# Kernel optimization log

Measured on AMD Instinct MI355X. Metric: run time of the kernel, lower is better.

Reference implementation:

```python
import jax, jax.numpy as jnp
import numpy as np

E = 64          # num_routed_experts
K = 6           # num_experts_per_token
NS = 2          # num_shared_experts
D = 512         # hidden_size
F = 512         # expert_intermediate_size = intermediate_size // 4


def setup_inputs() -> dict:
    key = jax.random.key(0)
    ks = jax.random.split(key, 8)
    s = 0.02
    return {
        "hidden_states": jax.random.normal(ks[0], (2, 1024, D), dtype=jnp.float32),
        "Wr": jax.random.normal(ks[1], (D, E), dtype=jnp.float32) * s,      # router
        "sWg": jax.random.normal(ks[2], (NS, D, F), dtype=jnp.float32) * s,  # shared gate_proj
        "sWu": jax.random.normal(ks[3], (NS, D, F), dtype=jnp.float32) * s,  # shared up_proj
        "sWd": jax.random.normal(ks[4], (NS, F, D), dtype=jnp.float32) * s,  # shared down_proj
        "Wg": jax.random.normal(ks[5], (E, D, F), dtype=jnp.float32) * s,    # routed gate_proj
        "Wu": jax.random.normal(ks[6], (E, D, F), dtype=jnp.float32) * s,    # routed up_proj
        "Wd": jax.random.normal(ks[7], (E, F, D), dtype=jnp.float32) * s,    # routed down_proj
    }


def _swiglu_ffn(x, wg, wu, wd):
    # x: (N, D); wg/wu: (D, F); wd: (F, D)
    return (jax.nn.silu(x @ wg) * (x @ wu)) @ wd


def reference(hidden_states, Wr, sWg, sWu, sWd, Wg, Wu, Wd):
    B, S, d = hidden_states.shape
    x = hidden_states.reshape(-1, d)  # (N, D)
    N = x.shape[0]

    # ---- shared experts (always on) ----
    shared = jnp.zeros_like(x)
    for e in range(NS):
        shared = shared + _swiglu_ffn(x, sWg[e], sWu[e], sWd[e])

    # ---- top-k router ----
    logits = x @ Wr                                   # (N, E)
    probs = jax.nn.softmax(logits, axis=-1)
    top_w, top_i = jax.lax.top_k(probs, K)            # (N, K)
    top_w = top_w / jnp.sum(top_w, axis=-1, keepdims=True)  # renormalize
    gate = jnp.zeros((N, E), dtype=x.dtype).at[jnp.arange(N)[:, None], top_i].set(top_w)

    # ---- routed experts: per-expert FFN, combined with sparse gate ----
    routed = jnp.zeros_like(x)
    for e in range(E):
        routed = routed + _swiglu_ffn(x, Wg[e], Wu[e], Wd[e]) * gate[:, e:e + 1]

    out = (shared + routed + x).reshape(B, S, d)
    return out
```

## Files before the change

### kernel.cpp

```cpp
#include <hip/hip_runtime.h>

#define N_TOK 2048
#define DD 512
#define FF 512
#define EE 64
#define TK 6
#define NG 66
#define RSLOT 12288
#define NSLOT 16384
#define BM 64
#define BN 64
#define NT 16
#define MAXT 320

typedef float f32x4 __attribute__((ext_vector_type(4)));
typedef __bf16 bf16x8 __attribute__((ext_vector_type(8)));

__device__ __forceinline__ unsigned cvtpk(float lo, float hi) {
  unsigned r;
  asm("v_cvt_pk_bf16_f32 %0, %1, %2" : "=v"(r) : "v"(lo), "v"(hi));
  return r;
}

__device__ __forceinline__ bf16x8 pack8(f32x4 a, f32x4 b) {
  union { unsigned u[4]; bf16x8 v; } r;
  r.u[0] = cvtpk(a[0], a[1]); r.u[1] = cvtpk(a[2], a[3]);
  r.u[2] = cvtpk(b[0], b[1]); r.u[3] = cvtpk(b[2], b[3]);
  return r.v;
}

__device__ __forceinline__ void gll16(const void* g, void* l) {
  __builtin_amdgcn_global_load_lds(
      (const __attribute__((address_space(1))) unsigned int*)g,
      (__attribute__((address_space(3))) unsigned int*)l, 16, 0, 0);
}

__global__ __launch_bounds__(256) void router_k(
    const float* __restrict__ x, const float* __restrict__ Wr,
    int* __restrict__ top_i, float* __restrict__ top_w, int* __restrict__ cnt) {
  __shared__ float xs[16 * 512];
  __shared__ float part[4][16][64];
  int tid = threadIdx.x, lane = tid & 63, w = tid >> 6;
  int t0 = blockIdx.x * 16;

  const f32x4* xin = (const f32x4*)(x + (size_t)t0 * DD);
  f32x4* xs4 = (f32x4*)xs;
#pragma unroll
  for (int i = 0; i < 8; ++i) xs4[i * 256 + tid] = xin[i * 256 + tid];
  __syncthreads();

  float acc[16];
#pragma unroll
  for (int t = 0; t < 16; ++t) acc[t] = 0.f;
  for (int kk = 0; kk < 32; ++kk) {
    int k = w * 128 + kk * 4;
    float w0 = Wr[(size_t)(k + 0) * EE + lane];
    float w1 = Wr[(size_t)(k + 1) * EE + lane];
    float w2 = Wr[(size_t)(k + 2) * EE + lane];
    float w3 = Wr[(size_t)(k + 3) * EE + lane];
#pragma unroll
    for (int t = 0; t < 16; ++t) {
      f32x4 xv = *(const f32x4*)&xs[t * 512 + k];
      acc[t] = fmaf(xv[0], w0, acc[t]);
      acc[t] = fmaf(xv[1], w1, acc[t]);
      acc[t] = fmaf(xv[2], w2, acc[t]);
      acc[t] = fmaf(xv[3], w3, acc[t]);
    }
  }
#pragma unroll
  for (int t = 0; t < 16; ++t) part[w][t][lane] = acc[t];
  __syncthreads();

#pragma unroll
  for (int tt = 0; tt < 4; ++tt) {
    int t = w * 4 + tt;
    float l0 = part[0][t][lane] + part[1][t][lane] + part[2][t][lane] + part[3][t][lane];
    float m = l0;
#pragma unroll
    for (int s = 32; s; s >>= 1) m = fmaxf(m, __shfl_xor(m, s));
    float p = __expf(l0 - m);
    int wi[TK]; float wv[TK];
#pragma unroll
    for (int it = 0; it < TK; ++it) {
      float v = p;
#pragma unroll
      for (int s = 32; s; s >>= 1) v = fmaxf(v, __shfl_xor(v, s));
      unsigned long long b = __ballot(p == v);
      int idx = __ffsll((unsigned long long)b) - 1;
      wi[it] = idx; wv[it] = v;
      if (lane == idx) p = -1.f;
    }
    float wsum = 0.f;
#pragma unroll
    for (int it = 0; it < TK; ++it) wsum += wv[it];
    int tg = t0 + t;
    if (lane < TK) {
      int si = 0; float sv = 0.f;
#pragma unroll
      for (int it = 0; it < TK; ++it) if (lane == it) { si = wi[it]; sv = wv[it]; }
      top_i[tg * TK + lane] = si;
      top_w[tg * TK + lane] = sv / wsum;
      atomicAdd(&cnt[si], 1);
    }
  }
}

__global__ void offsets_k(const int* __restrict__ cnt, int* __restrict__ goff,
                          int* __restrict__ fill, int* __restrict__ wk_g,
                          int* __restrict__ wk_mt, int* __restrict__ nitems) {
  int i = threadIdx.x;
  fill[i] = 0;
  int c = cnt[i];
  int s = c;
#pragma unroll
  for (int d = 1; d < 64; d <<= 1) { int t = __shfl_up(s, d); if (i >= d) s += t; }
  goff[i] = s - c;
  if (i == 63) {
    goff[EE] = RSLOT;
    goff[EE + 1] = RSLOT + N_TOK;
    goff[EE + 2] = RSLOT + 2 * N_TOK;
  }
  int nt = (c + BM - 1) >> 6;
  int ts = nt;
#pragma unroll
  for (int d = 1; d < 64; d <<= 1) { int t = __shfl_up(ts, d); if (i >= d) ts += t; }
  int texcl = ts - nt;
  for (int t = 0; t < nt; ++t) { wk_g[texcl + t] = i; wk_mt[texcl + t] = t; }
  int tot = __shfl(ts, 63);
  wk_g[tot + i] = EE + (i >> 5);
  wk_mt[tot + i] = i & 31;
  if (i == 0) nitems[0] = tot + 64;
}

__global__ void scatter_k(const int* __restrict__ top_i, const float* __restrict__ top_w,
                          const int* __restrict__ goff, int* __restrict__ fill,
                          int* __restrict__ btok, float* __restrict__ bw) {
  int idx = blockIdx.x * blockDim.x + threadIdx.x;
  if (idx < RSLOT) {
    int e = top_i[idx];
    int pos = goff[e] + atomicAdd(&fill[e], 1);
    btok[pos] = idx / TK;
    bw[pos] = top_w[idx];
  } else if (idx < NSLOT) {
    int j = idx - RSLOT;
    btok[idx] = j & (N_TOK - 1);
    bw[idx] = 1.0f;
  }
}

__global__ void initout_k(const float* __restrict__ x, float* __restrict__ out, int n4) {
  int i = blockIdx.x * blockDim.x + threadIdx.x;
  if (i < n4) reinterpret_cast<f32x4*>(out)[i] = reinterpret_cast<const f32x4*>(x)[i];
}

__global__ __launch_bounds__(256) void gemm1_k(
    const float* __restrict__ x, const float* __restrict__ Wg, const float* __restrict__ Wu,
    const float* __restrict__ sWg, const float* __restrict__ sWu,
    const int* __restrict__ goff, const int* __restrict__ btok,
    const int* __restrict__ wk_g, const int* __restrict__ wk_mt,
    const int* __restrict__ nitems,
    short* __restrict__ H) {
  int item = blockIdx.y;
  if (item >= nitems[0]) return;
  int g = wk_g[item], mt = wk_mt[item];
  int s0g = goff[g], cnt = goff[g + 1] - s0g;
  int n0 = blockIdx.x * BN;
  const float* wgp = (g < EE) ? Wg + (size_t)g * DD * FF : sWg + (size_t)(g - EE) * DD * FF;
  const float* wup = (g < EE) ? Wu + (size_t)g * DD * FF : sWu + (size_t)(g - EE) * DD * FF;

  __shared__ __align__(16) float lds[2][6144];

  int tid = threadIdx.x;
  int lane = tid & 63;
  int w = tid >> 6;
  int wr = w >> 1, wc = w & 1;
  int lr = lane & 15, lgq = lane >> 4;
  int s0 = s0g + mt * BM;

  const float* sp[6];
  int ldsoff[6], strf[6];
#pragma unroll
  for (int q = 0; q < 6; ++q) {
    int c = w * 6 + q;
    ldsoff[q] = c * 256;
    if (c < 8) {
      int row = c * 8 + (lane >> 3);
      int tok = btok[s0 + row];
      sp[q] = x + (size_t)tok * DD + (((lane & 7) ^ (lane >> 3)) << 2);
      strf[q] = 32;
    } else if (c < 16) {
      int cc = c - 8;
      int krow = cc * 4 + (lane >> 4);
      int colf = ((((lane & 15) << 4) ^ (((cc >> 1) & 3) << 5)) >> 2);
      sp[q] = wgp + (size_t)krow * FF + n0 + colf;
      strf[q] = 32 * FF;
    } else {
      int cc = c - 16;
      int krow = cc * 4 + (lane >> 4);
      int colf = ((((lane & 15) << 4) ^ (((cc >> 1) & 3) << 5)) >> 2);
      sp[q] = wup + (size_t)krow * FF + n0 + colf;
      strf[q] = 32 * FF;
    }
  }

  f32x4 accg[2][2], accu[2][2];
#pragma unroll
  for (int i = 0; i < 2; ++i)
#pragma unroll
    for (int j = 0; j < 2; ++j) {
      accg[i][j] = f32x4{0.f, 0.f, 0.f, 0.f};
      accu[i][j] = f32x4{0.f, 0.f, 0.f, 0.f};
    }

  auto STAGE = [&](int b, int kt) {
#pragma unroll
    for (int q = 0; q < 6; ++q)
      gll16(sp[q] + (size_t)kt * strf[q], &lds[b][ldsoff[q]]);
  };
  auto COMPUTE = [&](int b) {
    const float* Am = &lds[b][0];
    const float* Gm = &lds[b][2048];
    const float* Um = &lds[b][4096];
    bf16x8 af[2], bg[2], bu[2];
#pragma unroll
    for (int i = 0; i < 2; ++i) {
      int row = wr * 32 + i * 16 + lr;
      int sw = (row & 7) << 2;
      f32x4 v0 = *(const f32x4*)&Am[row * 32 + ((lgq * 8) ^ sw)];
      f32x4 v1 = *(const f32x4*)&Am[row * 32 + ((lgq * 8 + 4) ^ sw)];
      af[i] = pack8(v0, v1);
    }
#pragma unroll
    for (int j = 0; j < 2; ++j) {
      int col = wc * 32 + j * 16 + lr;
      int cx = col ^ (lgq << 3);
      int kb = lgq * 8;
      f32x4 g0, g1, u0, u1;
#pragma unroll
      for (int i2 = 0; i2 < 4; ++i2) {
        g0[i2] = Gm[(kb + i2) * 64 + cx];
        g1[i2] = Gm[(kb + 4 + i2) * 64 + cx];
        u0[i2] = Um[(kb + i2) * 64 + cx];
        u1[i2] = Um[(kb + 4 + i2) * 64 + cx];
      }
      bg[j] = pack8(g0, g1);
      bu[j] = pack8(u0, u1);
    }
#pragma unroll
    for (int i = 0; i < 2; ++i)
#pragma unroll
      for (int j = 0; j < 2; ++j) {
        accg[i][j] = __builtin_amdgcn_mfma_f32_16x16x32_bf16(af[i], bg[j], accg[i][j], 0, 0, 0);
        accu[i][j] = __builtin_amdgcn_mfma_f32_16x16x32_bf16(af[i], bu[j], accu[i][j], 0, 0, 0);
      }
  };

  STAGE(0, 0);
  __syncthreads();
  int b = 0;
#pragma unroll 1
  for (int kt = 0; kt < NT; ++kt) {
    if (kt + 1 < NT) STAGE(b ^ 1, kt + 1);
    COMPUTE(b);
    __syncthreads();
    b ^= 1;
  }

#pragma unroll
  for (int i = 0; i < 2; ++i)
#pragma unroll
    for (int j = 0; j < 2; ++j)
#pragma unroll
      for (int r = 0; r < 4; ++r) {
        int mrow = wr * 32 + i * 16 + lgq * 4 + r;
        if (mt * BM + mrow < cnt) {
          float gg = accg[i][j][r];
          float uu = accu[i][j][r];
          float hv = (gg / (1.f + __expf(-gg))) * uu;
          int col = n0 + wc * 32 + j * 16 + lr;
          H[(size_t)(s0 + mrow) * FF + col] = (short)(cvtpk(hv, hv) & 0xffffu);
        }
      }
}

__global__ __launch_bounds__(256) void gemm2_k(
    const short* __restrict__ H, const float* __restrict__ Wd, const float* __restrict__ sWd,
    const int* __restrict__ goff, const int* __restrict__ btok, const float* __restrict__ bw,
    const int* __restrict__ wk_g, const int* __restrict__ wk_mt,
    const int* __restrict__ nitems,
    float* __restrict__ out) {
  int item = blockIdx.y;
  if (item >= nitems[0]) return;
  int g = wk_g[item], mt = wk_mt[item];
  int s0g = goff[g], cnt = goff[g + 1] - s0g;
  int n0 = blockIdx.x * BN;
  const float* wdp = (g < EE) ? Wd + (size_t)g * FF * DD : sWd + (size_t)(g - EE) * FF * DD;

  __shared__ __align__(16) short lds[2][6144];

  int tid = threadIdx.x;
  int lane = tid & 63;
  int w = tid >> 6;
  int wr = w >> 1, wc = w & 1;
  int lr = lane & 15, lgq = lane >> 4;
  int s0 = s0g + mt * BM;

  const char* sp[3];
  int ldsbyte[3], strb[3];
#pragma unroll
  for (int q = 0; q < 3; ++q) {
    int c = w * 3 + q;
    ldsbyte[q] = c * 1024;
    if (c < 4) {
      int row = c * 16 + (lane >> 2);
      int slot = s0 + row;
      sp[q] = (const char*)(H + (size_t)slot * FF + (((lane & 3) ^ ((lane >> 2) & 3)) << 3));
      strb[q] = 64;
    } else {
      int cc = c - 4;
      int krow = cc * 4 + (lane >> 4);
      int colf = ((((lane & 15) << 4) ^ (((cc >> 1) & 3) << 5)) >> 2);
      sp[q] = (const char*)(wdp + (size_t)krow * DD + n0 + colf);
      strb[q] = 32 * DD * 4;
    }
  }

  f32x4 acc[2][2];
#pragma unroll
  for (int i = 0; i < 2; ++i)
#pragma unroll
    for (int j = 0; j < 2; ++j) acc[i][j] = f32x4{0.f, 0.f, 0.f, 0.f};

  auto STAGE = [&](int b, int kt) {
#pragma unroll
    for (int q = 0; q < 3; ++q)
      gll16(sp[q] + (size_t)kt * strb[q], (char*)lds[b] + ldsbyte[q]);
  };
  auto COMPUTE = [&](int b) {
    const short* Hm = lds[b];
    const float* Bm = (const float*)(lds[b] + 2048);
    bf16x8 af[2], bd[2];
#pragma unroll
    for (int i = 0; i < 2; ++i) {
      int row = wr * 32 + i * 16 + lr;
      af[i] = *(const bf16x8*)&Hm[row * 32 + ((lgq * 8) ^ ((row & 3) << 3))];
    }
#pragma unroll
    for (int j = 0; j < 2; ++j) {
      int col = wc * 32 + j * 16 + lr;
      int cx = col ^ (lgq << 3);
      int kb = lgq * 8;
      f32x4 d0, d1;
#pragma unroll
      for (int i2 = 0; i2 < 4; ++i2) {
        d0[i2] = Bm[(kb + i2) * 64 + cx];
        d1[i2] = Bm[(kb + 4 + i2) * 64 + cx];
      }
      bd[j] = pack8(d0, d1);
    }
#pragma unroll
    for (int i = 0; i < 2; ++i)
#pragma unroll
      for (int j = 0; j < 2; ++j)
        acc[i][j] = __builtin_amdgcn_mfma_f32_16x16x32_bf16(af[i], bd[j], acc[i][j], 0, 0, 0);
  };

  STAGE(0, 0);
  __syncthreads();
  int b = 0;
#pragma unroll 1
  for (int kt = 0; kt < NT; ++kt) {
    if (kt + 1 < NT) STAGE(b ^ 1, kt + 1);
    COMPUTE(b);
    __syncthreads();
    b ^= 1;
  }

#pragma unroll
  for (int i = 0; i < 2; ++i)
#pragma unroll
    for (int r = 0; r < 4; ++r) {
      int mrow = wr * 32 + i * 16 + lgq * 4 + r;
      if (mt * BM + mrow < cnt) {
        int slot = s0 + mrow;
        int tok = btok[slot];
        float wv = bw[slot];
#pragma unroll
        for (int j = 0; j < 2; ++j) {
          int col = n0 + wc * 32 + j * 16 + lr;
          atomicAdd(&out[(size_t)tok * DD + col], acc[i][j][r] * wv);
        }
      }
    }
}

extern "C" void kernel_launch(void* const* d_in, const int* in_sizes, int n_in,
                              void* d_out, int out_size, void* d_ws, size_t ws_size,
                              hipStream_t stream) {
  const float* x   = (const float*)d_in[0];
  const float* Wr  = (const float*)d_in[1];
  const float* sWg = (const float*)d_in[2];
  const float* sWu = (const float*)d_in[3];
  const float* sWd = (const float*)d_in[4];
  const float* Wg  = (const float*)d_in[5];
  const float* Wu  = (const float*)d_in[6];
  const float* Wd  = (const float*)d_in[7];
  float* out = (float*)d_out;

  char* wsb = (char*)d_ws;
  size_t off = 0;
  short* H = (short*)(wsb + off);     off += (size_t)NSLOT * FF * 2;
  int*   top_i = (int*)(wsb + off);   off += (size_t)RSLOT * 4;
  float* top_w = (float*)(wsb + off); off += (size_t)RSLOT * 4;
  int*   btok = (int*)(wsb + off);    off += (size_t)NSLOT * 4;
  float* bwt  = (float*)(wsb + off);  off += (size_t)NSLOT * 4;
  int*   cnt  = (int*)(wsb + off);    off += 256;
  int*   fill = (int*)(wsb + off);    off += 256;
  int*   goff = (int*)(wsb + off);    off += 512;
  int*   wk_g = (int*)(wsb + off);    off += MAXT * 4;
  int*   wk_mt = (int*)(wsb + off);   off += MAXT * 4;
  int*   nitems = (int*)(wsb + off);  off += 256;

  hipMemsetAsync(cnt, 0, 256, stream);
  router_k<<<N_TOK / 16, 256, 0, stream>>>(x, Wr, top_i, top_w, cnt);
  offsets_k<<<1, 64, 0, stream>>>(cnt, goff, fill, wk_g, wk_mt, nitems);
  scatter_k<<<NSLOT / 256, 256, 0, stream>>>(top_i, top_w, goff, fill, btok, bwt);
  int n4 = out_size / 4;
  initout_k<<<(n4 + 255) / 256, 256, 0, stream>>>(x, out, n4);
  dim3 grid1(FF / BN, MAXT, 1);
  gemm1_k<<<grid1, 256, 0, stream>>>(x, Wg, Wu, sWg, sWu, goff, btok, wk_g, wk_mt, nitems, H);
  dim3 grid2(DD / BN, MAXT, 1);
  gemm2_k<<<grid2, 256, 0, stream>>>(H, Wd, sWd, goff, btok, bwt, wk_g, wk_mt, nitems, out);
}
```

Measured before the change: 196.9 us.

## Pre-convert weights and activations to transposed bf16 before grouped GEMMs

Adds per-call kernels that convert all expert weight matrices to bf16 in an N-major transposed layout, and the input x to bf16. The GEMM kernels then stage bf16 tiles directly into LDS with K=64 per stage and swizzled 16-byte reads, so the per-element fp32 loads and in-loop packing are gone. This halves GEMM operand bytes and simplifies the LDS fragment loads. In exchange, every call runs an extra pass that reads all ~200 MB of fp32 weights and writes 100 MB of bf16, which is likely to dominate the runtime.

```diff
diff --git a/kernel.cpp b/kernel.cpp
--- a/kernel.cpp
+++ b/kernel.cpp
@@ -10,8 +10,10 @@
 #define NSLOT 16384
 #define BM 64
 #define BN 64
-#define NT 16
+#define BK 64
+#define NKT 8
 #define MAXT 320
+#define MATSZ 262144
 
 typedef float f32x4 __attribute__((ext_vector_type(4)));
 typedef __bf16 bf16x8 __attribute__((ext_vector_type(8)));
@@ -22,17 +24,54 @@
   return r;
 }
 
-__device__ __forceinline__ bf16x8 pack8(f32x4 a, f32x4 b) {
-  union { unsigned u[4]; bf16x8 v; } r;
-  r.u[0] = cvtpk(a[0], a[1]); r.u[1] = cvtpk(a[2], a[3]);
-  r.u[2] = cvtpk(b[0], b[1]); r.u[3] = cvtpk(b[2], b[3]);
-  return r.v;
-}
-
 __device__ __forceinline__ void gll16(const void* g, void* l) {
   __builtin_amdgcn_global_load_lds(
       (const __attribute__((address_space(1))) unsigned int*)g,
       (__attribute__((address_space(3))) unsigned int*)l, 16, 0, 0);
+}
+
+__global__ __launch_bounds__(256) void convw_k(
+    const float* __restrict__ Wg, const float* __restrict__ Wu, const float* __restrict__ Wd,
+    const float* __restrict__ sWg, const float* __restrict__ sWu, const float* __restrict__ sWd,
+    short* __restrict__ Wt) {
+  __shared__ float T[128][68];
+  int y = blockIdx.y;
+  int kind = y / 66, idx = y % 66;
+  const float* src;
+  if (kind == 0)      src = (idx < EE) ? Wg + (size_t)idx * MATSZ : sWg + (size_t)(idx - EE) * MATSZ;
+  else if (kind == 1) src = (idx < EE) ? Wu + (size_t)idx * MATSZ : sWu + (size_t)(idx - EE) * MATSZ;
+  else                src = (idx < EE) ? Wd + (size_t)idx * MATSZ : sWd + (size_t)(idx - EE) * MATSZ;
+  short* dst = Wt + (size_t)y * MATSZ;
+  int dt = blockIdx.x & 3, ft = blockIdx.x >> 2;
+  int tid = threadIdx.x;
+  int r = tid >> 1, half = tid & 1;
+  const float* sp = src + (size_t)(dt * 128 + r) * 512 + ft * 64 + half * 32;
+#pragma unroll
+  for (int j = 0; j < 8; ++j)
+    *(f32x4*)&T[r][half * 32 + j * 4] = *(const f32x4*)(sp + j * 4);
+  __syncthreads();
+#pragma unroll
+  for (int it = 0; it < 4; ++it) {
+    int ch = tid + 256 * it;
+    int f = ch >> 4, dseg = ch & 15;
+    float a[8];
+#pragma unroll
+    for (int i = 0; i < 8; ++i) a[i] = T[dseg * 8 + i][f];
+    uint4 o;
+    o.x = cvtpk(a[0], a[1]); o.y = cvtpk(a[2], a[3]);
+    o.z = cvtpk(a[4], a[5]); o.w = cvtpk(a[6], a[7]);
+    *(uint4*)&dst[(size_t)(ft * 64 + f) * 512 + dt * 128 + dseg * 8] = o;
+  }
+}
+
+__global__ void convx_k(const float* __restrict__ x, short* __restrict__ Xb) {
+  int i = blockIdx.x * 256 + threadIdx.x;
+  const f32x4* p = (const f32x4*)(x + (size_t)i * 8);
+  f32x4 v0 = p[0], v1 = p[1];
+  uint4 o;
+  o.x = cvtpk(v0[0], v0[1]); o.y = cvtpk(v0[2], v0[3]);
+  o.z = cvtpk(v1[0], v1[1]); o.w = cvtpk(v1[2], v1[3]);
+  *(uint4*)&Xb[(size_t)i * 8] = o;
 }
 
 __global__ __launch_bounds__(256) void router_k(
@@ -42,13 +81,11 @@
   __shared__ float part[4][16][64];
   int tid = threadIdx.x, lane = tid & 63, w = tid >> 6;
   int t0 = blockIdx.x * 16;
-
   const f32x4* xin = (const f32x4*)(x + (size_t)t0 * DD);
   f32x4* xs4 = (f32x4*)xs;
 #pragma unroll
   for (int i = 0; i < 8; ++i) xs4[i * 256 + tid] = xin[i * 256 + tid];
   __syncthreads();
-
   float acc[16];
 #pragma unroll
   for (int t = 0; t < 16; ++t) acc[t] = 0.f;
@@ -70,7 +107,6 @@
 #pragma unroll
   for (int t = 0; t < 16; ++t) part[w][t][lane] = acc[t];
   __syncthreads();
-
 #pragma unroll
   for (int tt = 0; tt < 4; ++tt) {
     int t = w * 4 + tt;
@@ -154,52 +190,40 @@
 }
 
 __global__ __launch_bounds__(256) void gemm1_k(
-    const float* __restrict__ x, const float* __restrict__ Wg, const float* __restrict__ Wu,
-    const float* __restrict__ sWg, const float* __restrict__ sWu,
+    const short* __restrict__ Xb, const short* __restrict__ Wtg, const short* __restrict__ Wtu,
     const int* __restrict__ goff, const int* __restrict__ btok,
     const int* __restrict__ wk_g, const int* __restrict__ wk_mt,
-    const int* __restrict__ nitems,
-    short* __restrict__ H) {
+    const int* __restrict__ nitems, short* __restrict__ H) {
   int item = blockIdx.y;
   if (item >= nitems[0]) return;
   int g = wk_g[item], mt = wk_mt[item];
   int s0g = goff[g], cnt = goff[g + 1] - s0g;
   int n0 = blockIdx.x * BN;
-  const float* wgp = (g < EE) ? Wg + (size_t)g * DD * FF : sWg + (size_t)(g - EE) * DD * FF;
-  const float* wup = (g < EE) ? Wu + (size_t)g * DD * FF : sWu + (size_t)(g - EE) * DD * FF;
-
-  __shared__ __align__(16) float lds[2][6144];
-
-  int tid = threadIdx.x;
-  int lane = tid & 63;
-  int w = tid >> 6;
+  const short* gmat = Wtg + (size_t)g * MATSZ;
+  const short* umat = Wtu + (size_t)g * MATSZ;
+
+  __shared__ __align__(16) short lds[2][12288];
+
+  int tid = threadIdx.x, lane = tid & 63, w = tid >> 6;
   int wr = w >> 1, wc = w & 1;
   int lr = lane & 15, lgq = lane >> 4;
   int s0 = s0g + mt * BM;
 
-  const float* sp[6];
-  int ldsoff[6], strf[6];
+  const short* sp[6];
+  int ldst[6];
 #pragma unroll
   for (int q = 0; q < 6; ++q) {
     int c = w * 6 + q;
-    ldsoff[q] = c * 256;
+    ldst[q] = c * 512;
+    int rl = (c & 7) * 8 + (lane >> 3);
+    int u = (lane & 7) ^ (rl & 7);
     if (c < 8) {
-      int row = c * 8 + (lane >> 3);
-      int tok = btok[s0 + row];
-      sp[q] = x + (size_t)tok * DD + (((lane & 7) ^ (lane >> 3)) << 2);
-      strf[q] = 32;
+      int slot = (mt * BM + rl < cnt) ? s0 + rl : s0;
+      sp[q] = Xb + (size_t)btok[slot] * 512 + u * 8;
     } else if (c < 16) {
-      int cc = c - 8;
-      int krow = cc * 4 + (lane >> 4);
-      int colf = ((((lane & 15) << 4) ^ (((cc >> 1) & 3) << 5)) >> 2);
-      sp[q] = wgp + (size_t)krow * FF + n0 + colf;
-      strf[q] = 32 * FF;
+      sp[q] = gmat + (size_t)(n0 + rl) * 512 + u * 8;
     } else {
-      int cc = c - 16;
-      int krow = cc * 4 + (lane >> 4);
-      int colf = ((((lane & 15) << 4) ^ (((cc >> 1) & 3) << 5)) >> 2);
-      sp[q] = wup + (size_t)krow * FF + n0 + colf;
-      strf[q] = 32 * FF;
+      sp[q] = umat + (size_t)(n0 + rl) * 512 + u * 8;
     }
   }
 
@@ -214,53 +238,41 @@
 
   auto STAGE = [&](int b, int kt) {
 #pragma unroll
-    for (int q = 0; q < 6; ++q)
-      gll16(sp[q] + (size_t)kt * strf[q], &lds[b][ldsoff[q]]);
+    for (int q = 0; q < 6; ++q) gll16(sp[q] + kt * 64, &lds[b][ldst[q]]);
   };
   auto COMPUTE = [&](int b) {
-    const float* Am = &lds[b][0];
-    const float* Gm = &lds[b][2048];
-    const float* Um = &lds[b][4096];
-    bf16x8 af[2], bg[2], bu[2];
-#pragma unroll
-    for (int i = 0; i < 2; ++i) {
-      int row = wr * 32 + i * 16 + lr;
-      int sw = (row & 7) << 2;
-      f32x4 v0 = *(const f32x4*)&Am[row * 32 + ((lgq * 8) ^ sw)];
-      f32x4 v1 = *(const f32x4*)&Am[row * 32 + ((lgq * 8 + 4) ^ sw)];
-      af[i] = pack8(v0, v1);
-    }
-#pragma unroll
-    for (int j = 0; j < 2; ++j) {
-      int col = wc * 32 + j * 16 + lr;
-      int cx = col ^ (lgq << 3);
-      int kb = lgq * 8;
-      f32x4 g0, g1, u0, u1;
-#pragma unroll
-      for (int i2 = 0; i2 < 4; ++i2) {
-        g0[i2] = Gm[(kb + i2) * 64 + cx];
-        g1[i2] = Gm[(kb + 4 + i2) * 64 + cx];
-        u0[i2] = Um[(kb + i2) * 64 + cx];
-        u1[i2] = Um[(kb + 4 + i2) * 64 + cx];
-      }
-      bg[j] = pack8(g0, g1);
-      bu[j] = pack8(u0, u1);
-    }
-#pragma unroll
-    for (int i = 0; i < 2; ++i)
+    const short* L = lds[b];
+#pragma unroll
+    for (int ks = 0; ks < 2; ++ks) {
+      bf16x8 af[2], bg[2], bu[2];
+#pragma unroll
+      for (int i = 0; i < 2; ++i) {
+        int row = wr * 32 + i * 16 + lr;
+        af[i] = *(const bf16x8*)&L[row * 64 + (((ks * 4 + lgq) ^ (row & 7)) * 8)];
+      }
 #pragma unroll
       for (int j = 0; j < 2; ++j) {
-        accg[i][j] = __builtin_amdgcn_mfma_f32_16x16x32_bf16(af[i], bg[j], accg[i][j], 0, 0, 0);
-        accu[i][j] = __builtin_amdgcn_mfma_f32_16x16x32_bf16(af[i], bu[j], accu[i][j], 0, 0, 0);
-      }
+        int fr = wc * 32 + j * 16 + lr;
+        int o = fr * 64 + (((ks * 4 + lgq) ^ (fr & 7)) * 8);
+        bg[j] = *(const bf16x8*)&L[4096 + o];
+        bu[j] = *(const bf16x8*)&L[8192 + o];
+      }
+#pragma unroll
+      for (int i = 0; i < 2; ++i)
+#pragma unroll
+        for (int j = 0; j < 2; ++j) {
+          accg[i][j] = __builtin_amdgcn_mfma_f32_16x16x32_bf16(af[i], bg[j], accg[i][j], 0, 0, 0);
+          accu[i][j] = __builtin_amdgcn_mfma_f32_16x16x32_bf16(af[i], bu[j], accu[i][j], 0, 0, 0);
+        }
+    }
   };
 
   STAGE(0, 0);
   __syncthreads();
   int b = 0;
 #pragma unroll 1
-  for (int kt = 0; kt < NT; ++kt) {
-    if (kt + 1 < NT) STAGE(b ^ 1, kt + 1);
+  for (int kt = 0; kt < NKT; ++kt) {
+    if (kt + 1 < NKT) STAGE(b ^ 1, kt + 1);
     COMPUTE(b);
     __syncthreads();
     b ^= 1;
@@ -284,44 +296,37 @@
 }
 
 __global__ __launch_bounds__(256) void gemm2_k(
-    const short* __restrict__ H, const float* __restrict__ Wd, const float* __restrict__ sWd,
+    const short* __restrict__ H, const short* __restrict__ Wtd,
     const int* __restrict__ goff, const int* __restrict__ btok, const float* __restrict__ bw,
     const int* __restrict__ wk_g, const int* __restrict__ wk_mt,
-    const int* __restrict__ nitems,
-    float* __restrict__ out) {
+    const int* __restrict__ nitems, float* __restrict__ out) {
   int item = blockIdx.y;
   if (item >= nitems[0]) return;
   int g = wk_g[item], mt = wk_mt[item];
   int s0g = goff[g], cnt = goff[g + 1] - s0g;
   int n0 = blockIdx.x * BN;
-  const float* wdp = (g < EE) ? Wd + (size_t)g * FF * DD : sWd + (size_t)(g - EE) * FF * DD;
-
-  __shared__ __align__(16) short lds[2][6144];
-
-  int tid = threadIdx.x;
-  int lane = tid & 63;
-  int w = tid >> 6;
+  const short* dmat = Wtd + (size_t)g * MATSZ;
+
+  __shared__ __align__(16) short lds[2][8192];
+
+  int tid = threadIdx.x, lane = tid & 63, w = tid >> 6;
   int wr = w >> 1, wc = w & 1;
   int lr = lane & 15, lgq = lane >> 4;
   int s0 = s0g + mt * BM;
 
-  const char* sp[3];
-  int ldsbyte[3], strb[3];
-#pragma unroll
-  for (int q = 0; q < 3; ++q) {
-    int c = w * 3 + q;
-    ldsbyte[q] = c * 1024;
-    if (c < 4) {
-      int row = c * 16 + (lane >> 2);
-      int slot = s0 + row;
-      sp[q] = (const char*)(H + (size_t)slot * FF + (((lane & 3) ^ ((lane >> 2) & 3)) << 3));
-      strb[q] = 64;
+  const short* sp[4];
+  int ldst[4];
+#pragma unroll
+  for (int q = 0; q < 4; ++q) {
+    int c = w * 4 + q;
+    ldst[q] = c * 512;
+    int rl = (c & 7) * 8 + (lane >> 3);
+    int u = (lane & 7) ^ (rl & 7);
+    if (c < 8) {
+      int slot = (mt * BM + rl < cnt) ? s0 + rl : s0;
+      sp[q] = H + (size_t)slot * 512 + u * 8;
     } else {
-      int cc = c - 4;
-      int krow = cc * 4 + (lane >> 4);
-      int colf = ((((lane & 15) << 4) ^ (((cc >> 1) & 3) << 5)) >> 2);
-      sp[q] = (const char*)(wdp + (size_t)krow * DD + n0 + colf);
-      strb[q] = 32 * DD * 4;
+      sp[q] = dmat + (size_t)(n0 + rl) * 512 + u * 8;
     }
   }
 
@@ -333,44 +338,37 @@
 
   auto STAGE = [&](int b, int kt) {
 #pragma unroll
-    for (int q = 0; q < 3; ++q)
-      gll16(sp[q] + (size_t)kt * strb[q], (char*)lds[b] + ldsbyte[q]);
+    for (int q = 0; q < 4; ++q) gll16(sp[q] + kt * 64, &lds[b][ldst[q]]);
   };
   auto COMPUTE = [&](int b) {
-    const short* Hm = lds[b];
-    const float* Bm = (const float*)(lds[b] + 2048);
-    bf16x8 af[2], bd[2];
-#pragma unroll
-    for (int i = 0; i < 2; ++i) {
-      int row = wr * 32 + i * 16 + lr;
-      af[i] = *(const bf16x8*)&Hm[row * 32 + ((lgq * 8) ^ ((row & 3) << 3))];
-    }
-#pragma unroll
-    for (int j = 0; j < 2; ++j) {
-      int col = wc * 32 + j * 16 + lr;
-      int cx = col ^ (lgq << 3);
-      int kb = lgq * 8;
-      f32x4 d0, d1;
-#pragma unroll
-      for (int i2 = 0; i2 < 4; ++i2) {
-        d0[i2] = Bm[(kb + i2) * 64 + cx];
-        d1[i2] = Bm[(kb + 4 + i2) * 64 + cx];
-      }
-      bd[j] = pack8(d0, d1);
-    }
-#pragma unroll
-    for (int i = 0; i < 2; ++i)
-#pragma unroll
-      for (int j = 0; j < 2; ++j)
-        acc[i][j] = __builtin_amdgcn_mfma_f32_16x16x32_bf16(af[i], bd[j], acc[i][j], 0, 0, 0);
+    const short* L = lds[b];
+#pragma unroll
+    for (int ks = 0; ks < 2; ++ks) {
+      bf16x8 af[2], bd[2];
+#pragma unroll
+      for (int i = 0; i < 2; ++i) {
+        int row = wr * 32 + i * 16 + lr;
+        af[i] = *(const bf16x8*)&L[row * 64 + (((ks * 4 + lgq) ^ (row & 7)) * 8)];
+      }
+#pragma unroll
+      for (int j = 0; j < 2; ++j) {
+        int dr = wc * 32 + j * 16 + lr;
+        bd[j] = *(const bf16x8*)&L[4096 + dr * 64 + (((ks * 4 + lgq) ^ (dr & 7)) * 8)];
+      }
+#pragma unroll
+      for (int i = 0; i < 2; ++i)
+#pragma unroll
+        for (int j = 0; j < 2; ++j)
+          acc[i][j] = __builtin_amdgcn_mfma_f32_16x16x32_bf16(af[i], bd[j], acc[i][j], 0, 0, 0);
+    }
   };
 
   STAGE(0, 0);
   __syncthreads();
   int b = 0;
 #pragma unroll 1
-  for (int kt = 0; kt < NT; ++kt) {
-    if (kt + 1 < NT) STAGE(b ^ 1, kt + 1);
+  for (int kt = 0; kt < NKT; ++kt) {
+    if (kt + 1 < NKT) STAGE(b ^ 1, kt + 1);
     COMPUTE(b);
     __syncthreads();
     b ^= 1;
@@ -409,7 +407,9 @@
 
   char* wsb = (char*)d_ws;
   size_t off = 0;
-  short* H = (short*)(wsb + off);     off += (size_t)NSLOT * FF * 2;
+  short* Wt = (short*)(wsb + off);    off += (size_t)198 * MATSZ * 2;
+  short* H  = (short*)(wsb + off);    off += (size_t)NSLOT * FF * 2;
+  short* Xb = (short*)(wsb + off);    off += (size_t)N_TOK * DD * 2;
   int*   top_i = (int*)(wsb + off);   off += (size_t)RSLOT * 4;
   float* top_w = (float*)(wsb + off); off += (size_t)RSLOT * 4;
   int*   btok = (int*)(wsb + off);    off += (size_t)NSLOT * 4;
@@ -421,14 +421,20 @@
   int*   wk_mt = (int*)(wsb + off);   off += MAXT * 4;
   int*   nitems = (int*)(wsb + off);  off += 256;
 
+  const short* Wtg = Wt;
+  const short* Wtu = Wt + (size_t)66 * MATSZ;
+  const short* Wtd = Wt + (size_t)132 * MATSZ;
+
   hipMemsetAsync(cnt, 0, 256, stream);
+  convw_k<<<dim3(32, 198), 256, 0, stream>>>(Wg, Wu, Wd, sWg, sWu, sWd, Wt);
+  convx_k<<<512, 256, 0, stream>>>(x, Xb);
   router_k<<<N_TOK / 16, 256, 0, stream>>>(x, Wr, top_i, top_w, cnt);
   offsets_k<<<1, 64, 0, stream>>>(cnt, goff, fill, wk_g, wk_mt, nitems);
   scatter_k<<<NSLOT / 256, 256, 0, stream>>>(top_i, top_w, goff, fill, btok, bwt);
   int n4 = out_size / 4;
   initout_k<<<(n4 + 255) / 256, 256, 0, stream>>>(x, out, n4);
   dim3 grid1(FF / BN, MAXT, 1);
-  gemm1_k<<<grid1, 256, 0, stream>>>(x, Wg, Wu, sWg, sWu, goff, btok, wk_g, wk_mt, nitems, H);
+  gemm1_k<<<grid1, 256, 0, stream>>>(Xb, Wtg, Wtu, goff, btok, wk_g, wk_mt, nitems, H);
   dim3 grid2(DD / BN, MAXT, 1);
-  gemm2_k<<<grid2, 256, 0, stream>>>(H, Wd, sWd, goff, btok, bwt, wk_g, wk_mt, nitems, out);
-}
+  gemm2_k<<<grid2, 256, 0, stream>>>(H, Wtd, goff, btok, bwt, wk_g, wk_mt, nitems, out);
+}
```

New measurement: 235.6 us. +19.7%, slower.
